# Optimization experiments

Measured on AMD Instinct MI355X. Metric: run time of the kernel, lower is better.

The kernel has to match this reference:

```python
import jax, jax.numpy as jnp
import numpy as np

EPS = 1e-4  # SPDRectifiedLinear eigenvalue threshold
POOL = 17   # adaptive pool output size


def setup_inputs() -> dict:
    key = jax.random.key(0)
    ks = jax.random.split(key, 6)
    B, Cin, H, W = 32, 2048, 34, 34
    Cr = 256
    feat_dim = Cr * (Cr + 1) // 2  # 32896
    x = jax.random.normal(ks[0], (B, Cin, H, W), dtype=jnp.float32)
    W_red = jax.random.normal(ks[1], (Cr, Cin), dtype=jnp.float32) * (1.0 / np.sqrt(Cin))
    W1 = jax.random.normal(ks[2], (256, feat_dim), dtype=jnp.float32) * (1.0 / np.sqrt(feat_dim))
    b1 = jax.random.normal(ks[3], (256,), dtype=jnp.float32) * 0.01
    W2 = jax.random.normal(ks[4], (3, 256), dtype=jnp.float32) * (1.0 / np.sqrt(256.0))
    b2 = jax.random.normal(ks[5], (3,), dtype=jnp.float32) * 0.01
    return {"x": x, "W_red": W_red, "W1": W1, "b1": b1, "W2": W2, "b2": b2}


def reference(x, W_red, W1, b1, W2, b2):
    B, Cin, H, W = x.shape
    # AdaptiveAvgPool2d((17,17)) with H=W=34 is exactly a uniform 2x2 avg pool
    f = x.reshape(B, Cin, POOL, H // POOL, POOL, W // POOL).mean(axis=(3, 5))  # [B,Cin,17,17]
    # 1x1 conv (no bias) == channel-mixing matmul
    f = jnp.einsum('bchw,dc->bdhw', f, W_red)  # [B,Cr,17,17]
    Cr = f.shape[1]
    f = f.reshape(B, Cr, -1).transpose(0, 2, 1)  # [B, N=289, Cr]
    N = f.shape[1]
    # batch covariance over spatial positions (unbiased)
    xc = f - f.mean(axis=1, keepdims=True)
    cov = jnp.einsum('bnc,bnd->bcd', xc, xc) / (N - 1)  # [B,Cr,Cr] SPD
    # SPD ReLU (eigenvalue clamp at EPS) followed by SPD logmap (matrix log)
    # share one eigendecomposition: same eigenvectors for both ops
    w, v = jnp.linalg.eigh(cov)
    w = jnp.log(jnp.clip(w, EPS))
    cov = jnp.einsum('bic,bc,bjc->bij', v, w, v)  # log-mapped symmetric matrix
    # SPD flatten: upper triangle, off-diagonal scaled by sqrt(2)
    iu, ju = jnp.triu_indices(Cr)
    scale = jnp.where(iu == ju, 1.0, jnp.sqrt(2.0)).astype(cov.dtype)
    flat = cov[:, iu, ju] * scale  # [B, Cr*(Cr+1)/2]
    # classifier MLP
    h = jax.nn.relu(flat @ W1.T + b1)
    return h @ W2.T + b2  # [B, num_classes]
```

## Files before the change

kernel.cpp:

```cpp
#include <hip/hip_runtime.h>
#include <math.h>


#define SWEEPS 7
#define NROUNDS (SWEEPS * 15)

#define P_OFF     0
#define A_OFF     0
#define V_OFF     8388608
#define U_OFF     16777216
#define LOGW_OFF  17825792
#define MEAN_OFF  79691776
#define F_OFF     83558400
#define FLAT_OFF  83558400
#define PART_OFF  93519872
#define H_OFF     94568448
#define WS_REQUIRED 94601216

__device__ __forceinline__ void pair16(int r, int t, int& p, int& q) {
    if (t == 0) { p = 0; q = 1 + r; return; }
    int u = r + t; if (u >= 15) u -= 15;
    int v = r - t; if (v < 0) v += 15;
    p = 1 + u; q = 1 + v;
    if (p > q) { int w = p; p = q; q = w; }
}
__device__ __forceinline__ void pair32(int rr, int t, int& p, int& q) {
    if (t == 0) { p = 0; q = 1 + rr; return; }
    int u = rr + t; if (u >= 31) u -= 31;
    int v = rr - t; if (v < 0) v += 31;
    p = 1 + u; q = 1 + v;
    if (p > q) { int w = p; p = q; q = w; }
}

__global__ __launch_bounds__(256) void k_pool(const float* __restrict__ x, float* __restrict__ P) {
    int c = blockIdx.x, b = blockIdx.y;
    const float* xs = x + (size_t)(b * 2048 + c) * 1156;
    float* ps = P + (size_t)(b * 2048 + c) * 304;
    for (int n = threadIdx.x; n < 289; n += 256) {
        int i = n / 17, j = n % 17;
        int base = (2 * i) * 34 + 2 * j;
        ps[n] = 0.25f * (xs[base] + xs[base + 1] + xs[base + 34] + xs[base + 35]);
    }
}

__global__ __launch_bounds__(256) void k_gemm_red(const float* __restrict__ P,
                                                  const float* __restrict__ Wr,
                                                  float* __restrict__ f) {
    __shared__ float Wt[32][33];
    __shared__ float Pt[32][64];
    int nt = blockIdx.x, dt = blockIdx.y, b = blockIdx.z;
    int n0 = nt * 64, d0 = dt * 32;
    int tid = threadIdx.x;
    int ty = tid >> 4, tx = tid & 15;
    float acc[2][4] = {};
    for (int c0 = 0; c0 < 2048; c0 += 32) {
        __syncthreads();
        for (int idx = tid; idx < 32 * 32; idx += 256) {
            int r = idx >> 5, cc = idx & 31;
            Wt[r][cc] = Wr[(size_t)(d0 + r) * 2048 + c0 + cc];
        }
        for (int idx = tid; idx < 32 * 64; idx += 256) {
            int r = idx >> 6, cc = idx & 63;
            int n = n0 + cc;
            Pt[r][cc] = (n < 289) ? P[(size_t)(b * 2048 + c0 + r) * 304 + n] : 0.0f;
        }
        __syncthreads();
#pragma unroll
        for (int kk = 0; kk < 32; ++kk) {
            float a0 = Wt[ty * 2 + 0][kk], a1 = Wt[ty * 2 + 1][kk];
            float p0 = Pt[kk][tx * 4 + 0], p1 = Pt[kk][tx * 4 + 1];
            float p2 = Pt[kk][tx * 4 + 2], p3 = Pt[kk][tx * 4 + 3];
            acc[0][0] += a0 * p0; acc[0][1] += a0 * p1; acc[0][2] += a0 * p2; acc[0][3] += a0 * p3;
            acc[1][0] += a1 * p0; acc[1][1] += a1 * p1; acc[1][2] += a1 * p2; acc[1][3] += a1 * p3;
        }
    }
    for (int ii = 0; ii < 2; ++ii)
        for (int jj = 0; jj < 4; ++jj) {
            int d = d0 + ty * 2 + ii, n = n0 + tx * 4 + jj;
            if (n < 289) f[(size_t)(b * 256 + d) * 304 + n] = acc[ii][jj];
        }
}

__global__ __launch_bounds__(256) void k_mean(const float* __restrict__ f, float* __restrict__ mean) {
    int row = blockIdx.x * 4 + (threadIdx.x >> 6);
    int lane = threadIdx.x & 63;
    const float* fr = f + (size_t)row * 304;
    double s = 0.0;
    for (int n = lane; n < 289; n += 64) s += (double)fr[n];
    for (int off = 32; off; off >>= 1) s += __shfl_down(s, off);
    if (lane == 0) mean[row] = (float)(s / 289.0);
}

__global__ __launch_bounds__(256) void k_cov(const float* __restrict__ f,
                                             const float* __restrict__ mean,
                                             float* __restrict__ A) {
    __shared__ float Fi[32][33];
    __shared__ float Fj[32][33];
    int b = blockIdx.x, tp = blockIdx.y;
    int ti = (int)((sqrtf(8.0f * tp + 1.0f) - 1.0f) * 0.5f);
    while (ti * (ti + 1) / 2 > tp) --ti;
    while ((ti + 1) * (ti + 2) / 2 <= tp) ++ti;
    int tj = tp - ti * (ti + 1) / 2;
    int tid = threadIdx.x;
    int tyy = tid >> 4, txx = tid & 15;
    bool diag = (ti == tj);
    double acc[2][2] = {};
    for (int nc = 0; nc < 289; nc += 32) {
        __syncthreads();
        for (int idx = tid; idx < 32 * 32; idx += 256) {
            int r = idx >> 5, k = idx & 31;
            int n = nc + k;
            int d1 = ti * 32 + r;
            Fi[r][k] = (n < 289) ? f[(size_t)(b * 256 + d1) * 304 + n] - mean[b * 256 + d1] : 0.0f;
            if (!diag) {
                int d2 = tj * 32 + r;
                Fj[r][k] = (n < 289) ? f[(size_t)(b * 256 + d2) * 304 + n] - mean[b * 256 + d2] : 0.0f;
            }
        }
        __syncthreads();
        const float(*FJ)[33] = diag ? Fi : Fj;
#pragma unroll 8
        for (int kk = 0; kk < 32; ++kk) {
            float a0 = Fi[tyy * 2 + 0][kk], a1 = Fi[tyy * 2 + 1][kk];
            float c0 = FJ[txx * 2 + 0][kk], c1 = FJ[txx * 2 + 1][kk];
            acc[0][0] += (double)a0 * c0; acc[0][1] += (double)a0 * c1;
            acc[1][0] += (double)a1 * c0; acc[1][1] += (double)a1 * c1;
        }
    }
    for (int ii = 0; ii < 2; ++ii)
        for (int jj = 0; jj < 2; ++jj) {
            int i = ti * 32 + tyy * 2 + ii, j = tj * 32 + txx * 2 + jj;
            float v = (float)(acc[ii][jj] * (1.0 / 288.0));
            A[((size_t)b << 16) + i * 256 + j] = v;
            if (!diag) A[((size_t)b << 16) + j * 256 + i] = v;
        }
}

__global__ __launch_bounds__(256) void k_init_v(float* __restrict__ V) {
    int i = blockIdx.x, b = blockIdx.y, j = threadIdx.x;
    V[((size_t)b << 16) + i * 256 + j] = (i == j) ? 1.0f : 0.0f;
}

__global__ __launch_bounds__(256) void k_inner(const float* __restrict__ A,
                                               float* __restrict__ Ubuf, int r) {
    __shared__ float S[32][33], UU[32][33];
    __shared__ float cbuf[16], sbuf[16];
    __shared__ int pbuf[16], qbuf[16];
    __shared__ float rednorm[8];
    int g = blockIdx.x, b = blockIdx.y;
    int tid = threadIdx.x;
    int bp, bq; pair16(r, g, bp, bq);
    const float* Ab = A + ((size_t)b << 16);
    for (int e = tid; e < 1024; e += 256) {
        int i = e >> 5, j = e & 31;
        int ri = (i < 16) ? bp * 16 + i : bq * 16 + i - 16;
        int rj = (j < 16) ? bp * 16 + j : bq * 16 + j - 16;
        S[i][j] = Ab[ri * 256 + rj];
        UU[i][j] = (i == j) ? 1.0f : 0.0f;
    }
    __syncthreads();
    for (int sw = 0; sw < 6; ++sw) {
        float off = 0.0f, dia = 0.0f;
        for (int e = tid; e < 1024; e += 256) {
            int i = e >> 5, j = e & 31; float v = S[i][j];
            if (i == j) dia += v * v; else off += v * v;
        }
        for (int o = 32; o; o >>= 1) { off += __shfl_down(off, o); dia += __shfl_down(dia, o); }
        if ((tid & 63) == 0) { rednorm[tid >> 6] = off; rednorm[4 + (tid >> 6)] = dia; }
        __syncthreads();
        off = rednorm[0] + rednorm[1] + rednorm[2] + rednorm[3];
        dia = rednorm[4] + rednorm[5] + rednorm[6] + rednorm[7];
        __syncthreads();
        if (off <= 1e-13f * fmaxf(dia, 1e-30f)) break;
        for (int rr = 0; rr < 31; ++rr) {
            if (tid < 16) {
                int p, q; pair32(rr, tid, p, q);
                float app = S[p][p], aqq = S[q][q], apq = S[p][q];
                float c = 1.0f, s = 0.0f;
                if (apq * apq > 1e-36f) {
                    float tau = (aqq - app) / (2.0f * apq);
                    float t = 1.0f / (fabsf(tau) + sqrtf(1.0f + tau * tau));
                    if (tau < 0.0f) t = -t;
                    c = rsqrtf(1.0f + t * t); s = t * c;
                }
                cbuf[tid] = c; sbuf[tid] = s; pbuf[tid] = p; qbuf[tid] = q;
            }
            __syncthreads();
            {
                int i = tid & 31, t0 = (tid >> 5) * 2;
#pragma unroll
                for (int m = 0; m < 2; ++m) {
                    int t = t0 + m;
                    int p = pbuf[t], q = qbuf[t];
                    float c = cbuf[t], s = sbuf[t];
                    float x = S[i][p], y = S[i][q];
                    S[i][p] = c * x - s * y; S[i][q] = s * x + c * y;
                    x = UU[i][p]; y = UU[i][q];
                    UU[i][p] = c * x - s * y; UU[i][q] = s * x + c * y;
                }
            }
            __syncthreads();
            {
                int j = tid & 31, t0 = (tid >> 5) * 2;
#pragma unroll
                for (int m = 0; m < 2; ++m) {
                    int t = t0 + m;
                    int p = pbuf[t], q = qbuf[t];
                    float c = cbuf[t], s = sbuf[t];
                    float x = S[p][j], y = S[q][j];
                    S[p][j] = c * x - s * y; S[q][j] = s * x + c * y;
                }
            }
            __syncthreads();
        }
    }
    for (int e = tid; e < 1024; e += 256)
        Ubuf[(((size_t)b * 8 + g) << 10) + e] = UU[e >> 5][e & 31];
}

__global__ __launch_bounds__(64) void k_update(float* __restrict__ A, float* __restrict__ V,
                                               const float* __restrict__ Ubuf, int r) {
    __shared__ float U1[32][33], U2[32][33], TT[32][33];
    int task = blockIdx.x, b = blockIdx.y;
    int l = threadIdx.x;
    int lr = l >> 3, lc = l & 7;
    int a0 = lr * 4, c0 = lc * 4;
    if (task < 64) {
        int gk = task >> 3, gl = task & 7;
        int pk, qk, pl, ql;
        pair16(r, gk, pk, qk); pair16(r, gl, pl, ql);
        const float* Uk = Ubuf + (((size_t)b * 8 + gk) << 10);
        const float* Ul = Ubuf + (((size_t)b * 8 + gl) << 10);
        float* Ab = A + ((size_t)b << 16);
        for (int e = l; e < 1024; e += 64) {
            int i = e >> 5, j = e & 31;
            U1[i][j] = Uk[e];
            U2[i][j] = Ul[e];
            int ri = (i < 16) ? pk * 16 + i : qk * 16 + i - 16;
            int rj = (j < 16) ? pl * 16 + j : ql * 16 + j - 16;
            TT[i][j] = Ab[ri * 256 + rj];
        }
        __syncthreads();
        float acc[4][4] = {};
#pragma unroll 4
        for (int k = 0; k < 32; ++k) {
            float u0 = U1[k][a0], u1 = U1[k][a0 + 1], u2 = U1[k][a0 + 2], u3 = U1[k][a0 + 3];
            float t0 = TT[k][c0], t1 = TT[k][c0 + 1], t2 = TT[k][c0 + 2], t3 = TT[k][c0 + 3];
            acc[0][0] += u0 * t0; acc[0][1] += u0 * t1; acc[0][2] += u0 * t2; acc[0][3] += u0 * t3;
            acc[1][0] += u1 * t0; acc[1][1] += u1 * t1; acc[1][2] += u1 * t2; acc[1][3] += u1 * t3;
            acc[2][0] += u2 * t0; acc[2][1] += u2 * t1; acc[2][2] += u2 * t2; acc[2][3] += u2 * t3;
            acc[3][0] += u3 * t0; acc[3][1] += u3 * t1; acc[3][2] += u3 * t2; acc[3][3] += u3 * t3;
        }
        __syncthreads();
#pragma unroll
        for (int i = 0; i < 4; ++i)
#pragma unroll
            for (int j = 0; j < 4; ++j) TT[a0 + i][c0 + j] = acc[i][j];
        __syncthreads();
        float acc2[4][4] = {};
#pragma unroll 4
        for (int k = 0; k < 32; ++k) {
            float w0 = TT[a0][k], w1 = TT[a0 + 1][k], w2 = TT[a0 + 2][k], w3 = TT[a0 + 3][k];
            float u0 = U2[k][c0], u1 = U2[k][c0 + 1], u2 = U2[k][c0 + 2], u3 = U2[k][c0 + 3];
            acc2[0][0] += w0 * u0; acc2[0][1] += w0 * u1; acc2[0][2] += w0 * u2; acc2[0][3] += w0 * u3;
            acc2[1][0] += w1 * u0; acc2[1][1] += w1 * u1; acc2[1][2] += w1 * u2; acc2[1][3] += w1 * u3;
            acc2[2][0] += w2 * u0; acc2[2][1] += w2 * u1; acc2[2][2] += w2 * u2; acc2[2][3] += w2 * u3;
            acc2[3][0] += w3 * u0; acc2[3][1] += w3 * u1; acc2[3][2] += w3 * u2; acc2[3][3] += w3 * u3;
        }
#pragma unroll
        for (int i = 0; i < 4; ++i) {
            int ga = a0 + i; int ri = (ga < 16) ? pk * 16 + ga : qk * 16 + ga - 16;
#pragma unroll
            for (int j = 0; j < 4; ++j) {
                int gc = c0 + j; int rj = (gc < 16) ? pl * 16 + gc : ql * 16 + gc - 16;
                Ab[ri * 256 + rj] = acc2[i][j];
            }
        }
    } else {
        int t2 = task - 64;
        int rb = t2 >> 3, gl = t2 & 7;
        int pl, ql; pair16(r, gl, pl, ql);
        const float* Ul = Ubuf + (((size_t)b * 8 + gl) << 10);
        float* Vb = V + ((size_t)b << 16);
        for (int e = l; e < 1024; e += 64) {
            int i = e >> 5, j = e & 31;
            U2[i][j] = Ul[e];
            int rj = (j < 16) ? pl * 16 + j : ql * 16 + j - 16;
            TT[i][j] = Vb[(rb * 32 + i) * 256 + rj];
        }
        __syncthreads();
        float acc2[4][4] = {};
#pragma unroll 4
        for (int k = 0; k < 32; ++k) {
            float w0 = TT[a0][k], w1 = TT[a0 + 1][k], w2 = TT[a0 + 2][k], w3 = TT[a0 + 3][k];
            float u0 = U2[k][c0], u1 = U2[k][c0 + 1], u2 = U2[k][c0 + 2], u3 = U2[k][c0 + 3];
            acc2[0][0] += w0 * u0; acc2[0][1] += w0 * u1; acc2[0][2] += w0 * u2; acc2[0][3] += w0 * u3;
            acc2[1][0] += w1 * u0; acc2[1][1] += w1 * u1; acc2[1][2] += w1 * u2; acc2[1][3] += w1 * u3;
            acc2[2][0] += w2 * u0; acc2[2][1] += w2 * u1; acc2[2][2] += w2 * u2; acc2[2][3] += w2 * u3;
            acc2[3][0] += w3 * u0; acc2[3][1] += w3 * u1; acc2[3][2] += w3 * u2; acc2[3][3] += w3 * u3;
        }
#pragma unroll
        for (int i = 0; i < 4; ++i)
#pragma unroll
            for (int j = 0; j < 4; ++j) {
                int gc = c0 + j; int rj = (gc < 16) ? pl * 16 + gc : ql * 16 + gc - 16;
                Vb[(rb * 32 + a0 + i) * 256 + rj] = acc2[i][j];
            }
    }
}

__global__ __launch_bounds__(256) void k_logw(const float* __restrict__ A, float* __restrict__ logw) {
    int b = blockIdx.x, k = threadIdx.x;
    logw[b * 256 + k] = logf(fmaxf(A[((size_t)b << 16) + k * 257], 1e-4f));
}

__global__ __launch_bounds__(256) void k_vlogv(const float* __restrict__ V,
                                               const float* __restrict__ logw,
                                               float* __restrict__ flat) {
    __shared__ float Vi[32][33], Vjw[32][33];
    int t = blockIdx.x, b = blockIdx.y;
    int ti = 0;
    while (t >= 8 - ti) { t -= 8 - ti; ++ti; }
    int tj = ti + t;
    int tid = threadIdx.x;
    int ty = tid >> 4, tx = tid & 15;
    const float* Vb = V + ((size_t)b << 16);
    const float* wb = logw + b * 256;
    float acc[2][2] = {};
    for (int kc = 0; kc < 8; ++kc) {
        __syncthreads();
        for (int e = tid; e < 1024; e += 256) {
            int rr = e >> 5, cc = e & 31;
            Vi[rr][cc] = Vb[(ti * 32 + rr) * 256 + kc * 32 + cc];
            Vjw[rr][cc] = Vb[(tj * 32 + rr) * 256 + kc * 32 + cc] * wb[kc * 32 + cc];
        }
        __syncthreads();
#pragma unroll 8
        for (int k = 0; k < 32; ++k) {
            float a0 = Vi[ty * 2][k], a1 = Vi[ty * 2 + 1][k];
            float b0 = Vjw[tx * 2][k], b1 = Vjw[tx * 2 + 1][k];
            acc[0][0] += a0 * b0; acc[0][1] += a0 * b1;
            acc[1][0] += a1 * b0; acc[1][1] += a1 * b1;
        }
    }
    const float SQ2 = 1.41421356237309515f;
    float* flatb = flat + (size_t)b * 32896;
#pragma unroll
    for (int ii = 0; ii < 2; ++ii)
#pragma unroll
        for (int jj = 0; jj < 2; ++jj) {
            int gi = ti * 32 + ty * 2 + ii, gj = tj * 32 + tx * 2 + jj;
            if (gi <= gj) {
                int fidx = gi * 256 - gi * (gi - 1) / 2 + (gj - gi);
                flatb[fidx] = acc[ii][jj] * ((gi == gj) ? 1.0f : SQ2);
            }
        }
}

__global__ __launch_bounds__(256) void k_mlp1(const float* __restrict__ flat,
                                              const float* __restrict__ W1,
                                              float* __restrict__ partial) {
    __shared__ float Fl[32][65];
    __shared__ float Wl[32][65];
    int ec = blockIdx.x, jt = blockIdx.y;
    int tid = threadIdx.x;
    int e0 = ec * 1028;
    float acc[4] = {};
    for (int ch = 0; ch < 1028; ch += 64) {
        __syncthreads();
        for (int idx = tid; idx < 2048; idx += 256) {
            int row = idx >> 6, col = idx & 63;
            int e = ch + col;
            float fv = 0.0f, wv = 0.0f;
            if (e < 1028) {
                fv = flat[(size_t)row * 32896 + e0 + e];
                wv = W1[(size_t)(jt * 32 + row) * 32896 + e0 + e];
            }
            Fl[row][col] = fv; Wl[row][col] = wv;
        }
        __syncthreads();
#pragma unroll 4
        for (int ee = 0; ee < 64; ++ee) {
#pragma unroll
            for (int pp = 0; pp < 4; ++pp) {
                int pair = tid + pp * 256;
                acc[pp] += Wl[pair >> 5][ee] * Fl[pair & 31][ee];
            }
        }
    }
    for (int pp = 0; pp < 4; ++pp)
        partial[((size_t)(jt * 32 + ec) << 10) + tid + pp * 256] = acc[pp];
}

__global__ __launch_bounds__(1024) void k_mlp1red(const float* __restrict__ partial,
                                                  const float* __restrict__ b1,
                                                  float* __restrict__ h) {
    int jt = blockIdx.x, tid = threadIdx.x;
    float acc = 0.0f;
    for (int ec = 0; ec < 32; ++ec) acc += partial[((size_t)(jt * 32 + ec) << 10) + tid];
    int j = jt * 32 + (tid >> 5), bI = tid & 31;
    h[bI * 256 + j] = fmaxf(acc + b1[j], 0.0f);
}

__global__ __launch_bounds__(128) void k_mlp2(const float* __restrict__ h,
                                              const float* __restrict__ W2,
                                              const float* __restrict__ b2,
                                              float* __restrict__ out) {
    int tid = threadIdx.x;
    if (tid >= 96) return;
    int bI = tid / 3, cls = tid % 3;
    double acc = (double)b2[cls];
    for (int j = 0; j < 256; ++j) acc += (double)h[bI * 256 + j] * (double)W2[cls * 256 + j];
    out[tid] = (float)acc;
}

extern "C" void kernel_launch(void* const* d_in, const int* in_sizes, int n_in,
                              void* d_out, int out_size, void* d_ws, size_t ws_size,
                              hipStream_t stream) {
    const float* x  = (const float*)d_in[0];
    const float* Wr = (const float*)d_in[1];
    const float* W1 = (const float*)d_in[2];
    const float* b1 = (const float*)d_in[3];
    const float* W2 = (const float*)d_in[4];
    const float* b2 = (const float*)d_in[5];
    float* out = (float*)d_out;
    char* ws = (char*)d_ws;
    if (ws_size < (size_t)WS_REQUIRED) return;

    float* P    = (float*)(ws + P_OFF);
    float* A    = (float*)(ws + A_OFF);
    float* V    = (float*)(ws + V_OFF);
    float* Ubuf = (float*)(ws + U_OFF);
    float* logw = (float*)(ws + LOGW_OFF);
    float* mean = (float*)(ws + MEAN_OFF);
    float* f    = (float*)(ws + F_OFF);
    float* flat = (float*)(ws + FLAT_OFF);
    float* part = (float*)(ws + PART_OFF);
    float* h    = (float*)(ws + H_OFF);

    k_pool<<<dim3(2048, 32), 256, 0, stream>>>(x, P);
    k_gemm_red<<<dim3(5, 8, 32), 256, 0, stream>>>(P, Wr, f);
    k_mean<<<2048, 256, 0, stream>>>(f, mean);
    k_cov<<<dim3(32, 36), 256, 0, stream>>>(f, mean, A);
    k_init_v<<<dim3(256, 32), 256, 0, stream>>>(V);
    for (int r = 0; r < NROUNDS; ++r) {
        int rr = r % 15;
        k_inner<<<dim3(8, 32), 256, 0, stream>>>(A, Ubuf, rr);
        k_update<<<dim3(128, 32), 64, 0, stream>>>(A, V, Ubuf, rr);
    }
    k_logw<<<32, 256, 0, stream>>>(A, logw);
    k_vlogv<<<dim3(36, 32), 256, 0, stream>>>(V, logw, flat);
    k_mlp1<<<dim3(32, 8), 256, 0, stream>>>(flat, W1, part);
    k_mlp1red<<<8, 1024, 0, stream>>>(part, b1, h);
    k_mlp2<<<1, 128, 0, stream>>>(h, W2, b2, out);
}
```

Measured before the change: 12.70 ms.

## Shrink Jacobi inner kernel to one wavefront, skip converged block updates, vectorize LDS

The inner block-Jacobi kernel now runs as a single 64-thread wavefront. Its norm reduction becomes wave shuffles with no shared-memory barriers, and the p/q pairs are recomputed per thread instead of staged in shared memory. When a block pair needed no rotations it writes a flag, so the update kernel can skip A tiles and V row-blocks whose rotation is the identity. The update kernel also switches to float4 global and LDS loads and stores with padded rows. The single-wave inner kernel does four times more rotation work per thread, which may slow it during the early, unconverged sweeps.

```diff
diff --git a/kernel.cpp b/kernel.cpp
--- a/kernel.cpp
+++ b/kernel.cpp
@@ -9,7 +9,8 @@
 #define A_OFF     0
 #define V_OFF     8388608
 #define U_OFF     16777216
-#define LOGW_OFF  17825792
+#define FLAG_OFF  17825792
+#define LOGW_OFF  17826816
 #define MEAN_OFF  79691776
 #define F_OFF     83558400
 #define FLAT_OFF  83558400
@@ -141,17 +142,16 @@
     V[((size_t)b << 16) + i * 256 + j] = (i == j) ? 1.0f : 0.0f;
 }
 
-__global__ __launch_bounds__(256) void k_inner(const float* __restrict__ A,
-                                               float* __restrict__ Ubuf, int r) {
+__global__ __launch_bounds__(64) void k_inner(const float* __restrict__ A,
+                                              float* __restrict__ Ubuf,
+                                              int* __restrict__ flags, int r) {
     __shared__ float S[32][33], UU[32][33];
     __shared__ float cbuf[16], sbuf[16];
-    __shared__ int pbuf[16], qbuf[16];
-    __shared__ float rednorm[8];
     int g = blockIdx.x, b = blockIdx.y;
     int tid = threadIdx.x;
     int bp, bq; pair16(r, g, bp, bq);
     const float* Ab = A + ((size_t)b << 16);
-    for (int e = tid; e < 1024; e += 256) {
+    for (int e = tid; e < 1024; e += 64) {
         int i = e >> 5, j = e & 31;
         int ri = (i < 16) ? bp * 16 + i : bq * 16 + i - 16;
         int rj = (j < 16) ? bp * 16 + j : bq * 16 + j - 16;
@@ -159,19 +159,18 @@
         UU[i][j] = (i == j) ? 1.0f : 0.0f;
     }
     __syncthreads();
+    int didwork = 0;
     for (int sw = 0; sw < 6; ++sw) {
         float off = 0.0f, dia = 0.0f;
-        for (int e = tid; e < 1024; e += 256) {
+        for (int e = tid; e < 1024; e += 64) {
             int i = e >> 5, j = e & 31; float v = S[i][j];
             if (i == j) dia += v * v; else off += v * v;
         }
+#pragma unroll
         for (int o = 32; o; o >>= 1) { off += __shfl_down(off, o); dia += __shfl_down(dia, o); }
-        if ((tid & 63) == 0) { rednorm[tid >> 6] = off; rednorm[4 + (tid >> 6)] = dia; }
-        __syncthreads();
-        off = rednorm[0] + rednorm[1] + rednorm[2] + rednorm[3];
-        dia = rednorm[4] + rednorm[5] + rednorm[6] + rednorm[7];
-        __syncthreads();
+        off = __shfl(off, 0); dia = __shfl(dia, 0);
         if (off <= 1e-13f * fmaxf(dia, 1e-30f)) break;
+        didwork = 1;
         for (int rr = 0; rr < 31; ++rr) {
             if (tid < 16) {
                 int p, q; pair32(rr, tid, p, q);
@@ -183,15 +182,15 @@
                     if (tau < 0.0f) t = -t;
                     c = rsqrtf(1.0f + t * t); s = t * c;
                 }
-                cbuf[tid] = c; sbuf[tid] = s; pbuf[tid] = p; qbuf[tid] = q;
+                cbuf[tid] = c; sbuf[tid] = s;
             }
             __syncthreads();
             {
-                int i = tid & 31, t0 = (tid >> 5) * 2;
-#pragma unroll
-                for (int m = 0; m < 2; ++m) {
-                    int t = t0 + m;
-                    int p = pbuf[t], q = qbuf[t];
+                int i = tid & 31, tbase = (tid >> 5) * 8;
+#pragma unroll
+                for (int m = 0; m < 8; ++m) {
+                    int t = tbase + m;
+                    int p, q; pair32(rr, t, p, q);
                     float c = cbuf[t], s = sbuf[t];
                     float x = S[i][p], y = S[i][q];
                     S[i][p] = c * x - s * y; S[i][q] = s * x + c * y;
@@ -201,11 +200,11 @@
             }
             __syncthreads();
             {
-                int j = tid & 31, t0 = (tid >> 5) * 2;
-#pragma unroll
-                for (int m = 0; m < 2; ++m) {
-                    int t = t0 + m;
-                    int p = pbuf[t], q = qbuf[t];
+                int j = tid & 31, tbase = (tid >> 5) * 8;
+#pragma unroll
+                for (int m = 0; m < 8; ++m) {
+                    int t = tbase + m;
+                    int p, q; pair32(rr, t, p, q);
                     float c = cbuf[t], s = sbuf[t];
                     float x = S[p][j], y = S[q][j];
                     S[p][j] = c * x - s * y; S[q][j] = s * x + c * y;
@@ -214,98 +213,96 @@
             __syncthreads();
         }
     }
-    for (int e = tid; e < 1024; e += 256)
+    if (tid == 0) flags[b * 8 + g] = (didwork == 0);
+    for (int e = tid; e < 1024; e += 64)
         Ubuf[(((size_t)b * 8 + g) << 10) + e] = UU[e >> 5][e & 31];
 }
 
 __global__ __launch_bounds__(64) void k_update(float* __restrict__ A, float* __restrict__ V,
-                                               const float* __restrict__ Ubuf, int r) {
-    __shared__ float U1[32][33], U2[32][33], TT[32][33];
+                                               const float* __restrict__ Ubuf,
+                                               const int* __restrict__ flags, int r) {
+    __shared__ float U1[32][36], U2[32][36], TT[32][36];
     int task = blockIdx.x, b = blockIdx.y;
     int l = threadIdx.x;
     int lr = l >> 3, lc = l & 7;
     int a0 = lr * 4, c0 = lc * 4;
     if (task < 64) {
         int gk = task >> 3, gl = task & 7;
+        if (flags[b * 8 + gk] && flags[b * 8 + gl]) return;
         int pk, qk, pl, ql;
         pair16(r, gk, pk, qk); pair16(r, gl, pl, ql);
         const float* Uk = Ubuf + (((size_t)b * 8 + gk) << 10);
         const float* Ul = Ubuf + (((size_t)b * 8 + gl) << 10);
         float* Ab = A + ((size_t)b << 16);
-        for (int e = l; e < 1024; e += 64) {
-            int i = e >> 5, j = e & 31;
-            U1[i][j] = Uk[e];
-            U2[i][j] = Ul[e];
+        for (int e4 = l; e4 < 256; e4 += 64) {
+            int i = e4 >> 3, j = (e4 & 7) * 4;
+            *(float4*)&U1[i][j] = *(const float4*)(Uk + i * 32 + j);
+            *(float4*)&U2[i][j] = *(const float4*)(Ul + i * 32 + j);
             int ri = (i < 16) ? pk * 16 + i : qk * 16 + i - 16;
             int rj = (j < 16) ? pl * 16 + j : ql * 16 + j - 16;
-            TT[i][j] = Ab[ri * 256 + rj];
+            *(float4*)&TT[i][j] = *(const float4*)(Ab + ri * 256 + rj);
         }
         __syncthreads();
         float acc[4][4] = {};
 #pragma unroll 4
         for (int k = 0; k < 32; ++k) {
-            float u0 = U1[k][a0], u1 = U1[k][a0 + 1], u2 = U1[k][a0 + 2], u3 = U1[k][a0 + 3];
-            float t0 = TT[k][c0], t1 = TT[k][c0 + 1], t2 = TT[k][c0 + 2], t3 = TT[k][c0 + 3];
-            acc[0][0] += u0 * t0; acc[0][1] += u0 * t1; acc[0][2] += u0 * t2; acc[0][3] += u0 * t3;
-            acc[1][0] += u1 * t0; acc[1][1] += u1 * t1; acc[1][2] += u1 * t2; acc[1][3] += u1 * t3;
-            acc[2][0] += u2 * t0; acc[2][1] += u2 * t1; acc[2][2] += u2 * t2; acc[2][3] += u2 * t3;
-            acc[3][0] += u3 * t0; acc[3][1] += u3 * t1; acc[3][2] += u3 * t2; acc[3][3] += u3 * t3;
+            float4 u = *(const float4*)&U1[k][a0];
+            float4 t = *(const float4*)&TT[k][c0];
+            acc[0][0] += u.x * t.x; acc[0][1] += u.x * t.y; acc[0][2] += u.x * t.z; acc[0][3] += u.x * t.w;
+            acc[1][0] += u.y * t.x; acc[1][1] += u.y * t.y; acc[1][2] += u.y * t.z; acc[1][3] += u.y * t.w;
+            acc[2][0] += u.z * t.x; acc[2][1] += u.z * t.y; acc[2][2] += u.z * t.z; acc[2][3] += u.z * t.w;
+            acc[3][0] += u.w * t.x; acc[3][1] += u.w * t.y; acc[3][2] += u.w * t.z; acc[3][3] += u.w * t.w;
         }
         __syncthreads();
 #pragma unroll
         for (int i = 0; i < 4; ++i)
-#pragma unroll
-            for (int j = 0; j < 4; ++j) TT[a0 + i][c0 + j] = acc[i][j];
+            *(float4*)&TT[a0 + i][c0] = make_float4(acc[i][0], acc[i][1], acc[i][2], acc[i][3]);
         __syncthreads();
         float acc2[4][4] = {};
 #pragma unroll 4
         for (int k = 0; k < 32; ++k) {
+            float4 u = *(const float4*)&U2[k][c0];
             float w0 = TT[a0][k], w1 = TT[a0 + 1][k], w2 = TT[a0 + 2][k], w3 = TT[a0 + 3][k];
-            float u0 = U2[k][c0], u1 = U2[k][c0 + 1], u2 = U2[k][c0 + 2], u3 = U2[k][c0 + 3];
-            acc2[0][0] += w0 * u0; acc2[0][1] += w0 * u1; acc2[0][2] += w0 * u2; acc2[0][3] += w0 * u3;
-            acc2[1][0] += w1 * u0; acc2[1][1] += w1 * u1; acc2[1][2] += w1 * u2; acc2[1][3] += w1 * u3;
-            acc2[2][0] += w2 * u0; acc2[2][1] += w2 * u1; acc2[2][2] += w2 * u2; acc2[2][3] += w2 * u3;
-            acc2[3][0] += w3 * u0; acc2[3][1] += w3 * u1; acc2[3][2] += w3 * u2; acc2[3][3] += w3 * u3;
-        }
+            acc2[0][0] += w0 * u.x; acc2[0][1] += w0 * u.y; acc2[0][2] += w0 * u.z; acc2[0][3] += w0 * u.w;
+            acc2[1][0] += w1 * u.x; acc2[1][1] += w1 * u.y; acc2[1][2] += w1 * u.z; acc2[1][3] += w1 * u.w;
+            acc2[2][0] += w2 * u.x; acc2[2][1] += w2 * u.y; acc2[2][2] += w2 * u.z; acc2[2][3] += w2 * u.w;
+            acc2[3][0] += w3 * u.x; acc2[3][1] += w3 * u.y; acc2[3][2] += w3 * u.z; acc2[3][3] += w3 * u.w;
+        }
+        int rj = (c0 < 16) ? pl * 16 + c0 : ql * 16 + c0 - 16;
 #pragma unroll
         for (int i = 0; i < 4; ++i) {
             int ga = a0 + i; int ri = (ga < 16) ? pk * 16 + ga : qk * 16 + ga - 16;
-#pragma unroll
-            for (int j = 0; j < 4; ++j) {
-                int gc = c0 + j; int rj = (gc < 16) ? pl * 16 + gc : ql * 16 + gc - 16;
-                Ab[ri * 256 + rj] = acc2[i][j];
-            }
+            *(float4*)(Ab + ri * 256 + rj) = make_float4(acc2[i][0], acc2[i][1], acc2[i][2], acc2[i][3]);
         }
     } else {
         int t2 = task - 64;
         int rb = t2 >> 3, gl = t2 & 7;
+        if (flags[b * 8 + gl]) return;
         int pl, ql; pair16(r, gl, pl, ql);
         const float* Ul = Ubuf + (((size_t)b * 8 + gl) << 10);
         float* Vb = V + ((size_t)b << 16);
-        for (int e = l; e < 1024; e += 64) {
-            int i = e >> 5, j = e & 31;
-            U2[i][j] = Ul[e];
+        for (int e4 = l; e4 < 256; e4 += 64) {
+            int i = e4 >> 3, j = (e4 & 7) * 4;
+            *(float4*)&U2[i][j] = *(const float4*)(Ul + i * 32 + j);
             int rj = (j < 16) ? pl * 16 + j : ql * 16 + j - 16;
-            TT[i][j] = Vb[(rb * 32 + i) * 256 + rj];
+            *(float4*)&TT[i][j] = *(const float4*)(Vb + (rb * 32 + i) * 256 + rj);
         }
         __syncthreads();
         float acc2[4][4] = {};
 #pragma unroll 4
         for (int k = 0; k < 32; ++k) {
+            float4 u = *(const float4*)&U2[k][c0];
             float w0 = TT[a0][k], w1 = TT[a0 + 1][k], w2 = TT[a0 + 2][k], w3 = TT[a0 + 3][k];
-            float u0 = U2[k][c0], u1 = U2[k][c0 + 1], u2 = U2[k][c0 + 2], u3 = U2[k][c0 + 3];
-            acc2[0][0] += w0 * u0; acc2[0][1] += w0 * u1; acc2[0][2] += w0 * u2; acc2[0][3] += w0 * u3;
-            acc2[1][0] += w1 * u0; acc2[1][1] += w1 * u1; acc2[1][2] += w1 * u2; acc2[1][3] += w1 * u3;
-            acc2[2][0] += w2 * u0; acc2[2][1] += w2 * u1; acc2[2][2] += w2 * u2; acc2[2][3] += w2 * u3;
-            acc2[3][0] += w3 * u0; acc2[3][1] += w3 * u1; acc2[3][2] += w3 * u2; acc2[3][3] += w3 * u3;
-        }
+            acc2[0][0] += w0 * u.x; acc2[0][1] += w0 * u.y; acc2[0][2] += w0 * u.z; acc2[0][3] += w0 * u.w;
+            acc2[1][0] += w1 * u.x; acc2[1][1] += w1 * u.y; acc2[1][2] += w1 * u.z; acc2[1][3] += w1 * u.w;
+            acc2[2][0] += w2 * u.x; acc2[2][1] += w2 * u.y; acc2[2][2] += w2 * u.z; acc2[2][3] += w2 * u.w;
+            acc2[3][0] += w3 * u.x; acc2[3][1] += w3 * u.y; acc2[3][2] += w3 * u.z; acc2[3][3] += w3 * u.w;
+        }
+        int rj = (c0 < 16) ? pl * 16 + c0 : ql * 16 + c0 - 16;
 #pragma unroll
         for (int i = 0; i < 4; ++i)
-#pragma unroll
-            for (int j = 0; j < 4; ++j) {
-                int gc = c0 + j; int rj = (gc < 16) ? pl * 16 + gc : ql * 16 + gc - 16;
-                Vb[(rb * 32 + a0 + i) * 256 + rj] = acc2[i][j];
-            }
+            *(float4*)(Vb + (rb * 32 + a0 + i) * 256 + rj) =
+                make_float4(acc2[i][0], acc2[i][1], acc2[i][2], acc2[i][3]);
     }
 }
 
@@ -431,6 +428,7 @@
     float* A    = (float*)(ws + A_OFF);
     float* V    = (float*)(ws + V_OFF);
     float* Ubuf = (float*)(ws + U_OFF);
+    int*   flags= (int*)  (ws + FLAG_OFF);
     float* logw = (float*)(ws + LOGW_OFF);
     float* mean = (float*)(ws + MEAN_OFF);
     float* f    = (float*)(ws + F_OFF);
@@ -445,8 +443,8 @@
     k_init_v<<<dim3(256, 32), 256, 0, stream>>>(V);
     for (int r = 0; r < NROUNDS; ++r) {
         int rr = r % 15;
-        k_inner<<<dim3(8, 32), 256, 0, stream>>>(A, Ubuf, rr);
-        k_update<<<dim3(128, 32), 64, 0, stream>>>(A, V, Ubuf, rr);
+        k_inner<<<dim3(8, 32), 64, 0, stream>>>(A, Ubuf, flags, rr);
+        k_update<<<dim3(128, 32), 64, 0, stream>>>(A, V, Ubuf, flags, rr);
     }
     k_logw<<<32, 256, 0, stream>>>(A, logw);
     k_vlogv<<<dim3(36, 32), 256, 0, stream>>>(V, logw, flat);
```

Measured after the change: 23.13 ms. +82.1%, slower.
